# Performance work log

Hardware: AMD Instinct MI355X
Metric: run time of the kernel (lower is better)

Reference implementation:

```python
import jax, jax.numpy as jnp
import numpy as np

USER = 100000
ITEM = 100000
LATDIM = 64
ETYPE = 8
GNN_LAYERS = 2
HYPER_NUM = 128
N_EDGES = 100000


def setup_inputs() -> dict:
    key = jax.random.key(0)
    ks = jax.random.split(key, 7)
    # xavier-ish scaled params
    uEmbeds = jax.random.normal(ks[0], (USER, LATDIM), dtype=jnp.float32) * 0.05
    iEmbeds = jax.random.normal(ks[1], (ITEM, LATDIM), dtype=jnp.float32) * 0.05
    edgeTrans = jax.random.normal(ks[2], (ETYPE, LATDIM, LATDIM), dtype=jnp.float32) * 0.1
    src = jax.random.randint(ks[3], (N_EDGES,), 0, USER, dtype=jnp.int64 if jax.config.jax_enable_x64 else jnp.int32)
    tgt = jax.random.randint(ks[4], (N_EDGES,), 0, ITEM, dtype=src.dtype)
    val = jax.random.randint(ks[5], (N_EDGES,), 0, ETYPE, dtype=src.dtype)
    hyper = jax.random.normal(ks[6], (N_EDGES, HYPER_NUM), dtype=jnp.float32)
    return {"uEmbeds": uEmbeds, "iEmbeds": iEmbeds, "edgeTrans": edgeTrans,
            "hyper": hyper, "src": src, "tgt": tgt, "val": val}


def _hgnn_layer(edgeEmbeds, hyper):
    act = lambda x: jax.nn.leaky_relu(x, 0.5)
    # [d, H] = embeds^T @ hyper
    hyperEmbeds = act(jnp.einsum('ed,eh->dh', edgeEmbeds, hyper))
    # [E, d] = (hyperEmbeds @ hyper^T)^T
    nodeEmbeds = act(jnp.einsum('eh,dh->ed', hyper, hyperEmbeds))
    return nodeEmbeds


def reference(uEmbeds, iEmbeds, edgeTrans, hyper, src, tgt, val):
    srcE = uEmbeds[src]                       # [E, d] gather
    trans = edgeTrans[val]                    # [E, d, d] gather (large)
    # per-edge row-vector x matrix, then elementwise mult with tgt embeds
    edgeEmbeds = jnp.einsum('ed,edk->ek', srcE, trans) * iEmbeds[tgt]  # [E, d]
    for _ in range(GNN_LAYERS):
        edgeEmbeds = _hgnn_layer(edgeEmbeds, hyper) + edgeEmbeds
    srcOut = jax.ops.segment_sum(edgeEmbeds, src, num_segments=USER)  # sparse.sum over dim 1
    tgtOut = jax.ops.segment_sum(edgeEmbeds, tgt, num_segments=ITEM)  # sparse.sum over dim 0
    return (srcOut, tgtOut)
```

## Files before the change

### kernel.cpp

```cpp
#include <hip/hip_runtime.h>

#define E_N     100000
#define USER_N  100000
#define NROW    200000
#define NB_ACC  256
#define BIN_CAP 16384
#define E_PAD   114688
#define ACC_NCH 7
#define ACC_CHUNK 64
#define BUCKET_CAP 16
#define NB_INIT 782

typedef __bf16 bf16x8 __attribute__((ext_vector_type(8)));
typedef __bf16 bf16x4 __attribute__((ext_vector_type(4)));
typedef float  f32x4  __attribute__((ext_vector_type(4)));

__device__ __forceinline__ float leaky(float x) { return x > 0.f ? x : 0.5f * x; }

__global__ void initKernel(int* __restrict__ cnt, int* __restrict__ cnt8,
                           const float* __restrict__ T, __bf16* __restrict__ Tt) {
  const int b = blockIdx.x;
  const int i = b * 256 + threadIdx.x;
  if (i < NROW + 2) cnt[i] = 0;
  if (i < 8) cnt8[i] = 0;
  if (b < 8) {
    const float* Tv = T + (size_t)b * 4096;
    __bf16* Tb = Tt + (size_t)b * 4096;
    for (int idx = threadIdx.x; idx < 4096; idx += 256) {
      const int d = idx >> 6, k = idx & 63;
      Tb[k * 64 + d] = (__bf16)Tv[idx];
    }
  }
}

__global__ void binKernel(const int* __restrict__ val, const int* __restrict__ src,
                          const int* __restrict__ tgt,
                          int* __restrict__ perm, int* __restrict__ permSrc,
                          int* __restrict__ permTgt,
                          int* __restrict__ cnt8, int* __restrict__ cnt,
                          int* __restrict__ list) {
  __shared__ int lh[8], lbase[8];
  const int tid = threadIdx.x;
  if (tid < 8) lh[tid] = 0;
  __syncthreads();
  const int e = blockIdx.x * 256 + tid;
  int v = -1, slot = 0, s = 0, t = 0;
  if (e < E_N) {
    v = val[e]; s = src[e]; t = tgt[e];
    slot = atomicAdd(&lh[v], 1);
    const int ps = atomicAdd(&cnt[s], 1);
    if (ps < BUCKET_CAP) list[(size_t)s * BUCKET_CAP + ps] = e;
    const int pt = atomicAdd(&cnt[USER_N + t], 1);
    if (pt < BUCKET_CAP) list[(size_t)(USER_N + t) * BUCKET_CAP + pt] = e;
  }
  __syncthreads();
  if (tid < 8) lbase[tid] = atomicAdd(&cnt8[tid], lh[tid]);
  __syncthreads();
  if (v >= 0) {
    const int p = v * BIN_CAP + lbase[v] + slot;
    perm[p] = e; permSrc[p] = s; permTgt[p] = t;
  }
}

__global__ void __launch_bounds__(256) convertHyperTKernel(const float* __restrict__ hyper,
                                                           __bf16* __restrict__ hyperT,
                                                           __bf16* __restrict__ hyperB) {
  __shared__ __bf16 sT[128][72];
  const int tid = threadIdx.x;
  const int e0 = blockIdx.x * 64;
  const int h = tid >> 1, eoff = (tid & 1) * 32;
  if (e0 >= E_N) {
    const float4 z = make_float4(0.f, 0.f, 0.f, 0.f);
    #pragma unroll
    for (int q = 0; q < 4; ++q)
      *(float4*)((char*)(hyperT + (size_t)h * E_PAD + e0 + eoff) + q * 16) = z;
    return;
  }
  #pragma unroll
  for (int r = 0; r < 8; ++r) {
    const int idx = r * 256 + tid;
    const int e = idx >> 5, h4 = (idx & 31) * 4;
    float4 v = make_float4(0.f, 0.f, 0.f, 0.f);
    if (e0 + e < E_N) {
      v = *(const float4*)(hyper + (size_t)(e0 + e) * 128 + h4);
      bf16x4 pk;
      pk[0] = (__bf16)v.x; pk[1] = (__bf16)v.y; pk[2] = (__bf16)v.z; pk[3] = (__bf16)v.w;
      *(bf16x4*)(hyperB + (size_t)(e0 + e) * 128 + h4) = pk;
    }
    sT[h4 + 0][e] = (__bf16)v.x; sT[h4 + 1][e] = (__bf16)v.y;
    sT[h4 + 2][e] = (__bf16)v.z; sT[h4 + 3][e] = (__bf16)v.w;
  }
  __syncthreads();
  #pragma unroll
  for (int q = 0; q < 8; ++q) {
    const bf16x4 v = *(const bf16x4*)&sT[h][eoff + q * 4];
    *(bf16x4*)(hyperT + (size_t)h * E_PAD + e0 + eoff + q * 4) = v;
  }
}

__global__ void __launch_bounds__(256) stageAMfmaKernel(
    const float* __restrict__ uE, const float* __restrict__ iE, const __bf16* __restrict__ Tt,
    const int* __restrict__ permSrc, const int* __restrict__ permTgt,
    const int* __restrict__ perm, const int* __restrict__ cnt8,
    float* __restrict__ edge) {
  __shared__ float sC[4][16][68];
  const int v  = blockIdx.y;
  const int nE = min(cnt8[v], BIN_CAP);
  const int tid  = threadIdx.x;
  const int lane = tid & 63;
  const int wave = tid >> 6;
  const int l16 = lane & 15, quad = lane >> 4;
  const int wbase = blockIdx.x * 256 + wave * 64;
  if (wbase >= nE) return;

  bf16x8 Bf[2][4];
  #pragma unroll
  for (int kc = 0; kc < 2; ++kc)
    #pragma unroll
    for (int nt = 0; nt < 4; ++nt)
      Bf[kc][nt] = *(const bf16x8*)(Tt + (size_t)v * 4096 + (nt * 16 + l16) * 64 + kc * 32 + quad * 8);

  int sI[4], tI[4], eI[4];
  #pragma unroll
  for (int s = 0; s < 4; ++s) {
    const int eoffS = wbase + s * 16;
    const bool lv = (eoffS + l16 < nE);
    const int p = v * BIN_CAP + (lv ? eoffS + l16 : 0);
    sI[s] = permSrc[p]; tI[s] = permTgt[p]; eI[s] = perm[p];
  }

  float4 f0[4][2], f1[4][2];
  #pragma unroll
  for (int s = 0; s < 4; ++s)
    #pragma unroll
    for (int kc = 0; kc < 2; ++kc) {
      const float* ap = uE + (size_t)sI[s] * 64 + kc * 32 + quad * 8;
      f0[s][kc] = *(const float4*)ap;
      f1[s][kc] = *(const float4*)(ap + 4);
    }

  #pragma unroll
  for (int pr = 0; pr < 2; ++pr) {
    f32x4 acc[2][4];
    #pragma unroll
    for (int sh = 0; sh < 2; ++sh)
      #pragma unroll
      for (int nt = 0; nt < 4; ++nt) acc[sh][nt] = (f32x4){0.f, 0.f, 0.f, 0.f};
    #pragma unroll
    for (int sh = 0; sh < 2; ++sh) {
      const int s = pr * 2 + sh;
      #pragma unroll
      for (int kc = 0; kc < 2; ++kc) {
        bf16x8 a;
        a[0] = (__bf16)f0[s][kc].x; a[1] = (__bf16)f0[s][kc].y;
        a[2] = (__bf16)f0[s][kc].z; a[3] = (__bf16)f0[s][kc].w;
        a[4] = (__bf16)f1[s][kc].x; a[5] = (__bf16)f1[s][kc].y;
        a[6] = (__bf16)f1[s][kc].z; a[7] = (__bf16)f1[s][kc].w;
        #pragma unroll
        for (int nt = 0; nt < 4; ++nt)
          acc[sh][nt] = __builtin_amdgcn_mfma_f32_16x16x32_bf16(a, Bf[kc][nt], acc[sh][nt], 0, 0, 0);
      }
    }
    #pragma unroll
    for (int sh = 0; sh < 2; ++sh) {
      const int s = pr * 2 + sh;
      const int eoffS = wbase + s * 16;
      #pragma unroll
      for (int nt = 0; nt < 4; ++nt)
        #pragma unroll
        for (int reg = 0; reg < 4; ++reg)
          sC[wave][quad * 4 + reg][nt * 16 + l16] = acc[sh][nt][reg];
      const int r  = lane >> 2;
      const int c0 = (lane & 3) * 4;
      const int tj = __shfl(tI[s], r, 64);
      const int gj = __shfl(eI[s], r, 64);
      if (eoffS + r < nE) {
        #pragma unroll
        for (int q = 0; q < 4; ++q) {
          const int c = c0 + q * 16;
          const float4 cv = *(const float4*)&sC[wave][r][c];
          const float4 iv = *(const float4*)(iE + (size_t)tj * 64 + c);
          float4 rr;
          rr.x = cv.x * iv.x; rr.y = cv.y * iv.y;
          rr.z = cv.z * iv.z; rr.w = cv.w * iv.w;
          *(float4*)(edge + (size_t)gj * 64 + c) = rr;
        }
      }
    }
  }
}

__global__ void __launch_bounds__(512) hyperAccumMfmaKernel(
    const float* __restrict__ edge, const __bf16* __restrict__ hyperT,
    float* __restrict__ partials) {
  __shared__ __bf16 sE[2][64][72];
  const int tid  = threadIdx.x;
  const int lane = tid & 63;
  const int wave = tid >> 6;
  const int l16 = lane & 15, quad = lane >> 4;
  const int e0base = blockIdx.x * (ACC_NCH * ACC_CHUNK);
  const int d  = tid & 63;
  const int eg = tid >> 6;

  float rv[8];
  auto gload = [&](int c) {
    const int ebase = e0base + c * ACC_CHUNK + eg * 8;
    const float* p = edge + (size_t)ebase * 64 + d;
    if (ebase + 8 <= E_N) {
      #pragma unroll
      for (int i = 0; i < 8; ++i) rv[i] = p[i * 64];
    } else {
      #pragma unroll
      for (int i = 0; i < 8; ++i) rv[i] = (ebase + i < E_N) ? p[i * 64] : 0.f;
    }
  };
  auto swrite = [&](int b) {
    bf16x8 pk;
    #pragma unroll
    for (int i = 0; i < 8; ++i) pk[i] = (__bf16)rv[i];
    *(bf16x8*)&sE[b][d][eg * 8] = pk;
  };

  f32x4 acc[4];
  #pragma unroll
  for (int dt = 0; dt < 4; ++dt) acc[dt] = (f32x4){0.f, 0.f, 0.f, 0.f};

  gload(0); swrite(0);
  __syncthreads();
  for (int c = 0; c < ACC_NCH; ++c) {
    const int nb = c & 1;
    if (c + 1 < ACC_NCH) gload(c + 1);
    #pragma unroll
    for (int ks = 0; ks < 2; ++ks) {
      const int eoff = c * ACC_CHUNK + ks * 32 + quad * 8;
      const bf16x8 B = *(const bf16x8*)(hyperT + (size_t)(wave * 16 + l16) * E_PAD + e0base + eoff);
      bf16x8 A[4];
      #pragma unroll
      for (int dt = 0; dt < 4; ++dt)
        A[dt] = *(const bf16x8*)&sE[nb][dt * 16 + l16][ks * 32 + quad * 8];
      #pragma unroll
      for (int dt = 0; dt < 4; ++dt)
        acc[dt] = __builtin_amdgcn_mfma_f32_16x16x32_bf16(A[dt], B, acc[dt], 0, 0, 0);
    }
    if (c + 1 < ACC_NCH) {
      __syncthreads();
      swrite(nb ^ 1);
      __syncthreads();
    }
  }
  float* pp = partials + (size_t)blockIdx.x * 8192;
  const int h = wave * 16 + l16;
  #pragma unroll
  for (int dt = 0; dt < 4; ++dt)
    #pragma unroll
    for (int reg = 0; reg < 4; ++reg) {
      const int dd = dt * 16 + quad * 4 + reg;
      pp[dd * 128 + h] = acc[dt][reg];
    }
}

__global__ void __launch_bounds__(256) reduceKernel(const float* __restrict__ partials,
                                                    __bf16* __restrict__ HEtT) {
  __shared__ float sd[8][33];
  const int tid = threadIdx.x;
  const int o = blockIdx.x * 32 + (tid & 31);
  const int g = tid >> 5;
  float s = 0.f;
  #pragma unroll 4
  for (int b = g * 32; b < (g + 1) * 32; ++b) s += partials[(size_t)b * 8192 + o];
  sd[g][tid & 31] = s;
  __syncthreads();
  if (tid < 32) {
    float t = 0.f;
    #pragma unroll
    for (int k = 0; k < 8; ++k) t += sd[k][tid];
    HEtT[blockIdx.x * 32 + tid] = (__bf16)leaky(t);
  }
}

__global__ void __launch_bounds__(256) nodeUpdateMfmaKernel(
    const __bf16* __restrict__ HEtT, const __bf16* __restrict__ hyperB,
    float* __restrict__ edge) {
  const int tid  = threadIdx.x;
  const int lane = tid & 63;
  const int wave = tid >> 6;
  const int l16 = lane & 15, quad = lane >> 4;
  bf16x8 Bf[4][4];
  #pragma unroll
  for (int kc = 0; kc < 4; ++kc)
    #pragma unroll
    for (int dt = 0; dt < 4; ++dt)
      Bf[kc][dt] = *(const bf16x8*)(HEtT + (dt * 16 + l16) * 128 + kc * 32 + quad * 8);
  const int wv = blockIdx.x * 4 + wave;
  for (int t = wv; t < E_N / 16; t += 2048) {
    const int e0 = t * 16;
    bf16x8 A[4];
    #pragma unroll
    for (int kc = 0; kc < 4; ++kc)
      A[kc] = *(const bf16x8*)(hyperB + (size_t)(e0 + l16) * 128 + kc * 32 + quad * 8);
    f32x4 acc[4];
    #pragma unroll
    for (int dt = 0; dt < 4; ++dt) acc[dt] = (f32x4){0.f, 0.f, 0.f, 0.f};
    #pragma unroll
    for (int kc = 0; kc < 4; ++kc)
      #pragma unroll
      for (int dt = 0; dt < 4; ++dt)
        acc[dt] = __builtin_amdgcn_mfma_f32_16x16x32_bf16(A[kc], Bf[kc][dt], acc[dt], 0, 0, 0);
    #pragma unroll
    for (int dt = 0; dt < 4; ++dt) {
      const int d = dt * 16 + l16;
      #pragma unroll
      for (int reg = 0; reg < 4; ++reg) {
        const int e = e0 + quad * 4 + reg;
        float* ep = edge + (size_t)e * 64 + d;
        *ep = *ep + leaky(acc[dt][reg]);
      }
    }
  }
}

__global__ void gatherSumKernel(const float* __restrict__ edge,
                                const int* __restrict__ cnt,
                                const int* __restrict__ list,
                                float* __restrict__ out) {
  const int tid = threadIdx.x;
  const int sub = tid & 15;
  const int grpInWave = (tid >> 4) & 3;
  const int gid = blockIdx.x * 16 + (tid >> 4);
  const int nG = gridDim.x * 16;
  for (int r = gid; r < NROW; r += nG) {
    const int n = min(cnt[r], BUCKET_CAP);
    int eL = (sub < n) ? list[(size_t)r * BUCKET_CAP + sub] : 0;
    float4 acc = make_float4(0.f, 0.f, 0.f, 0.f);
    for (int i = 0; i < n; ++i) {
      const int e = __shfl(eL, grpInWave * 16 + i, 64);
      const float4 v = *(const float4*)(edge + (size_t)e * 64 + sub * 4);
      acc.x += v.x; acc.y += v.y; acc.z += v.z; acc.w += v.w;
    }
    *(float4*)(out + (size_t)r * 64 + sub * 4) = acc;
  }
}

extern "C" void kernel_launch(void* const* d_in, const int* in_sizes, int n_in,
                              void* d_out, int out_size, void* d_ws, size_t ws_size,
                              hipStream_t stream) {
  const float* uE    = (const float*)d_in[0];
  const float* iE    = (const float*)d_in[1];
  const float* T     = (const float*)d_in[2];
  const float* hyper = (const float*)d_in[3];
  const int*   src   = (const int*)d_in[4];
  const int*   tgt   = (const int*)d_in[5];
  const int*   val   = (const int*)d_in[6];
  float* out = (float*)d_out;
  float* ws  = (float*)d_ws;

  float*  edge     = ws;
  float*  partials = ws + 6400000;
  __bf16* HEtT     = (__bf16*)(ws + 6400000 + 4194304 + 65536);
  int* perm    = (int*)partials;
  int* permSrc = perm + 8 * BIN_CAP;
  int* permTgt = permSrc + 8 * BIN_CAP;
  int* cnt8    = permTgt + 8 * BIN_CAP;
  int* cnt  = (int*)(ws + 6400000 + 4194304 + 65536 + 4096);
  int* list = cnt + (NROW + 4);
  __bf16* hyperT = (__bf16*)(ws + 15136256);
  __bf16* hyperB = (__bf16*)(ws + 22476288);
  __bf16* Tt     = (__bf16*)(ws + 28876288);

  initKernel<<<NB_INIT, 256, 0, stream>>>(cnt, cnt8, T, Tt);
  binKernel<<<(E_N + 255) / 256, 256, 0, stream>>>(val, src, tgt, perm, permSrc, permTgt, cnt8, cnt, list);
  convertHyperTKernel<<<E_PAD / 64, 256, 0, stream>>>(hyper, hyperT, hyperB);
  stageAMfmaKernel<<<dim3(BIN_CAP / 256, 8), 256, 0, stream>>>(uE, iE, Tt, permSrc, permTgt, perm, cnt8, edge);

  for (int layer = 0; layer < 2; ++layer) {
    hyperAccumMfmaKernel<<<NB_ACC, 512, 0, stream>>>(edge, hyperT, partials);
    reduceKernel<<<256, 256, 0, stream>>>(partials, HEtT);
    nodeUpdateMfmaKernel<<<512, 256, 0, stream>>>(HEtT, hyperB, edge);
  }

  gatherSumKernel<<<12500, 256, 0, stream>>>(edge, cnt, list, out);
}
```

Before: 283.5 us.

## Fuse per-layer hypergraph kernels into one cooperative kernel with grid syncs

```diff
diff --git a/kernel.cpp b/kernel.cpp
--- a/kernel.cpp
+++ b/kernel.cpp
@@ -1,4 +1,7 @@
 #include <hip/hip_runtime.h>
+#include <hip/hip_cooperative_groups.h>
+
+namespace cg = cooperative_groups;
 
 #define E_N     100000
 #define USER_N  100000
@@ -190,132 +193,131 @@
   }
 }
 
-__global__ void __launch_bounds__(512) hyperAccumMfmaKernel(
-    const float* __restrict__ edge, const __bf16* __restrict__ hyperT,
-    float* __restrict__ partials) {
+__global__ void __launch_bounds__(512, 2) gnnFusedKernel(
+    const __bf16* __restrict__ hyperT, const __bf16* __restrict__ hyperB,
+    float* __restrict__ edge, float* __restrict__ partials, __bf16* __restrict__ HEtT) {
+  cg::grid_group grid = cg::this_grid();
   __shared__ __bf16 sE[2][64][72];
+  __shared__ float sd[16][33];
   const int tid  = threadIdx.x;
   const int lane = tid & 63;
   const int wave = tid >> 6;
   const int l16 = lane & 15, quad = lane >> 4;
-  const int e0base = blockIdx.x * (ACC_NCH * ACC_CHUNK);
   const int d  = tid & 63;
   const int eg = tid >> 6;
-
-  float rv[8];
-  auto gload = [&](int c) {
-    const int ebase = e0base + c * ACC_CHUNK + eg * 8;
-    const float* p = edge + (size_t)ebase * 64 + d;
-    if (ebase + 8 <= E_N) {
-      #pragma unroll
-      for (int i = 0; i < 8; ++i) rv[i] = p[i * 64];
-    } else {
-      #pragma unroll
-      for (int i = 0; i < 8; ++i) rv[i] = (ebase + i < E_N) ? p[i * 64] : 0.f;
-    }
-  };
-  auto swrite = [&](int b) {
-    bf16x8 pk;
-    #pragma unroll
-    for (int i = 0; i < 8; ++i) pk[i] = (__bf16)rv[i];
-    *(bf16x8*)&sE[b][d][eg * 8] = pk;
-  };
-
-  f32x4 acc[4];
-  #pragma unroll
-  for (int dt = 0; dt < 4; ++dt) acc[dt] = (f32x4){0.f, 0.f, 0.f, 0.f};
-
-  gload(0); swrite(0);
-  __syncthreads();
-  for (int c = 0; c < ACC_NCH; ++c) {
-    const int nb = c & 1;
-    if (c + 1 < ACC_NCH) gload(c + 1);
-    #pragma unroll
-    for (int ks = 0; ks < 2; ++ks) {
-      const int eoff = c * ACC_CHUNK + ks * 32 + quad * 8;
-      const bf16x8 B = *(const bf16x8*)(hyperT + (size_t)(wave * 16 + l16) * E_PAD + e0base + eoff);
-      bf16x8 A[4];
+  const int e0base = blockIdx.x * (ACC_NCH * ACC_CHUNK);
+
+  for (int layer = 0; layer < 2; ++layer) {
+    {
+      float rv[8];
+      auto gload = [&](int c) {
+        const int ebase = e0base + c * ACC_CHUNK + eg * 8;
+        const float* p = edge + (size_t)ebase * 64 + d;
+        if (ebase + 8 <= E_N) {
+          #pragma unroll
+          for (int i = 0; i < 8; ++i) rv[i] = p[i * 64];
+        } else {
+          #pragma unroll
+          for (int i = 0; i < 8; ++i) rv[i] = (ebase + i < E_N) ? p[i * 64] : 0.f;
+        }
+      };
+      auto swrite = [&](int b) {
+        bf16x8 pk;
+        #pragma unroll
+        for (int i = 0; i < 8; ++i) pk[i] = (__bf16)rv[i];
+        *(bf16x8*)&sE[b][d][eg * 8] = pk;
+      };
+
+      f32x4 acc[4];
+      #pragma unroll
+      for (int dt = 0; dt < 4; ++dt) acc[dt] = (f32x4){0.f, 0.f, 0.f, 0.f};
+
+      __syncthreads();
+      gload(0); swrite(0);
+      __syncthreads();
+      for (int c = 0; c < ACC_NCH; ++c) {
+        const int nb = c & 1;
+        if (c + 1 < ACC_NCH) gload(c + 1);
+        #pragma unroll
+        for (int ks = 0; ks < 2; ++ks) {
+          const int eoff = c * ACC_CHUNK + ks * 32 + quad * 8;
+          const bf16x8 B = *(const bf16x8*)(hyperT + (size_t)(wave * 16 + l16) * E_PAD + e0base + eoff);
+          bf16x8 A[4];
+          #pragma unroll
+          for (int dt = 0; dt < 4; ++dt)
+            A[dt] = *(const bf16x8*)&sE[nb][dt * 16 + l16][ks * 32 + quad * 8];
+          #pragma unroll
+          for (int dt = 0; dt < 4; ++dt)
+            acc[dt] = __builtin_amdgcn_mfma_f32_16x16x32_bf16(A[dt], B, acc[dt], 0, 0, 0);
+        }
+        if (c + 1 < ACC_NCH) {
+          __syncthreads();
+          swrite(nb ^ 1);
+          __syncthreads();
+        }
+      }
+      float* pp = partials + (size_t)blockIdx.x * 8192;
+      const int h = wave * 16 + l16;
       #pragma unroll
       for (int dt = 0; dt < 4; ++dt)
-        A[dt] = *(const bf16x8*)&sE[nb][dt * 16 + l16][ks * 32 + quad * 8];
-      #pragma unroll
-      for (int dt = 0; dt < 4; ++dt)
-        acc[dt] = __builtin_amdgcn_mfma_f32_16x16x32_bf16(A[dt], B, acc[dt], 0, 0, 0);
-    }
-    if (c + 1 < ACC_NCH) {
+        #pragma unroll
+        for (int reg = 0; reg < 4; ++reg) {
+          const int dd = dt * 16 + quad * 4 + reg;
+          pp[dd * 128 + h] = acc[dt][reg];
+        }
+    }
+    grid.sync();
+    {
+      const int o = blockIdx.x * 32 + (tid & 31);
+      const int g = tid >> 5;
+      float s = 0.f;
+      #pragma unroll 4
+      for (int b = g * 16; b < (g + 1) * 16; ++b) s += partials[(size_t)b * 8192 + o];
+      sd[g][tid & 31] = s;
       __syncthreads();
-      swrite(nb ^ 1);
-      __syncthreads();
-    }
-  }
-  float* pp = partials + (size_t)blockIdx.x * 8192;
-  const int h = wave * 16 + l16;
-  #pragma unroll
-  for (int dt = 0; dt < 4; ++dt)
-    #pragma unroll
-    for (int reg = 0; reg < 4; ++reg) {
-      const int dd = dt * 16 + quad * 4 + reg;
-      pp[dd * 128 + h] = acc[dt][reg];
-    }
-}
-
-__global__ void __launch_bounds__(256) reduceKernel(const float* __restrict__ partials,
-                                                    __bf16* __restrict__ HEtT) {
-  __shared__ float sd[8][33];
-  const int tid = threadIdx.x;
-  const int o = blockIdx.x * 32 + (tid & 31);
-  const int g = tid >> 5;
-  float s = 0.f;
-  #pragma unroll 4
-  for (int b = g * 32; b < (g + 1) * 32; ++b) s += partials[(size_t)b * 8192 + o];
-  sd[g][tid & 31] = s;
-  __syncthreads();
-  if (tid < 32) {
-    float t = 0.f;
-    #pragma unroll
-    for (int k = 0; k < 8; ++k) t += sd[k][tid];
-    HEtT[blockIdx.x * 32 + tid] = (__bf16)leaky(t);
-  }
-}
-
-__global__ void __launch_bounds__(256) nodeUpdateMfmaKernel(
-    const __bf16* __restrict__ HEtT, const __bf16* __restrict__ hyperB,
-    float* __restrict__ edge) {
-  const int tid  = threadIdx.x;
-  const int lane = tid & 63;
-  const int wave = tid >> 6;
-  const int l16 = lane & 15, quad = lane >> 4;
-  bf16x8 Bf[4][4];
-  #pragma unroll
-  for (int kc = 0; kc < 4; ++kc)
-    #pragma unroll
-    for (int dt = 0; dt < 4; ++dt)
-      Bf[kc][dt] = *(const bf16x8*)(HEtT + (dt * 16 + l16) * 128 + kc * 32 + quad * 8);
-  const int wv = blockIdx.x * 4 + wave;
-  for (int t = wv; t < E_N / 16; t += 2048) {
-    const int e0 = t * 16;
-    bf16x8 A[4];
-    #pragma unroll
-    for (int kc = 0; kc < 4; ++kc)
-      A[kc] = *(const bf16x8*)(hyperB + (size_t)(e0 + l16) * 128 + kc * 32 + quad * 8);
-    f32x4 acc[4];
-    #pragma unroll
-    for (int dt = 0; dt < 4; ++dt) acc[dt] = (f32x4){0.f, 0.f, 0.f, 0.f};
-    #pragma unroll
-    for (int kc = 0; kc < 4; ++kc)
-      #pragma unroll
-      for (int dt = 0; dt < 4; ++dt)
-        acc[dt] = __builtin_amdgcn_mfma_f32_16x16x32_bf16(A[kc], Bf[kc][dt], acc[dt], 0, 0, 0);
-    #pragma unroll
-    for (int dt = 0; dt < 4; ++dt) {
-      const int d = dt * 16 + l16;
-      #pragma unroll
-      for (int reg = 0; reg < 4; ++reg) {
-        const int e = e0 + quad * 4 + reg;
-        float* ep = edge + (size_t)e * 64 + d;
-        *ep = *ep + leaky(acc[dt][reg]);
-      }
-    }
+      if (tid < 32) {
+        float t = 0.f;
+        #pragma unroll
+        for (int k = 0; k < 16; ++k) t += sd[k][tid];
+        HEtT[blockIdx.x * 32 + tid] = (__bf16)leaky(t);
+      }
+    }
+    grid.sync();
+    {
+      bf16x8 Bf[4][4];
+      #pragma unroll
+      for (int kc = 0; kc < 4; ++kc)
+        #pragma unroll
+        for (int dt = 0; dt < 4; ++dt)
+          Bf[kc][dt] = *(const bf16x8*)(HEtT + (dt * 16 + l16) * 128 + kc * 32 + quad * 8);
+      const int wv = blockIdx.x * 8 + wave;
+      for (int t = wv; t < E_N / 16; t += 2048) {
+        const int e0 = t * 16;
+        bf16x8 A[4];
+        #pragma unroll
+        for (int kc = 0; kc < 4; ++kc)
+          A[kc] = *(const bf16x8*)(hyperB + (size_t)(e0 + l16) * 128 + kc * 32 + quad * 8);
+        f32x4 acc[4];
+        #pragma unroll
+        for (int dt = 0; dt < 4; ++dt) acc[dt] = (f32x4){0.f, 0.f, 0.f, 0.f};
+        #pragma unroll
+        for (int kc = 0; kc < 4; ++kc)
+          #pragma unroll
+          for (int dt = 0; dt < 4; ++dt)
+            acc[dt] = __builtin_amdgcn_mfma_f32_16x16x32_bf16(A[kc], Bf[kc][dt], acc[dt], 0, 0, 0);
+        #pragma unroll
+        for (int dt = 0; dt < 4; ++dt) {
+          const int dd = dt * 16 + l16;
+          #pragma unroll
+          for (int reg = 0; reg < 4; ++reg) {
+            const int e = e0 + quad * 4 + reg;
+            float* ep = edge + (size_t)e * 64 + dd;
+            *ep = *ep + leaky(acc[dt][reg]);
+          }
+        }
+      }
+    }
+    if (layer == 0) grid.sync();
   }
 }
 
@@ -372,10 +374,9 @@
   convertHyperTKernel<<<E_PAD / 64, 256, 0, stream>>>(hyper, hyperT, hyperB);
   stageAMfmaKernel<<<dim3(BIN_CAP / 256, 8), 256, 0, stream>>>(uE, iE, Tt, permSrc, permTgt, perm, cnt8, edge);
 
-  for (int layer = 0; layer < 2; ++layer) {
-    hyperAccumMfmaKernel<<<NB_ACC, 512, 0, stream>>>(edge, hyperT, partials);
-    reduceKernel<<<256, 256, 0, stream>>>(partials, HEtT);
-    nodeUpdateMfmaKernel<<<512, 256, 0, stream>>>(HEtT, hyperB, edge);
+  {
+    void* args[] = {(void*)&hyperT, (void*)&hyperB, (void*)&edge, (void*)&partials, (void*)&HEtT};
+    hipLaunchCooperativeKernel((const void*)gnnFusedKernel, dim3(NB_ACC), dim3(512), args, 0, stream);
   }
 
   gatherSumKernel<<<12500, 256, 0, stream>>>(edge, cnt, list, out);
```

Measured after the change: 467.7 us. 1.65x slower.
